# Optimization experiments

Hardware: AMD Instinct MI355X
Metric: run time of the kernel (lower is better)

## Reference

```python
import jax, jax.numpy as jnp
import numpy as np

FM = 80            # feature_maps
N_ROUNDS = 32
NORM_EPS = 1e-3
LOSS_EPS = 1e-8


def _relu6(x):
    return jnp.clip(x, 0.0, 6.0)


def _norm(x):
    # tf.nn.moments over axis 0 + batch_normalization (no scale/offset)
    mean = jnp.mean(x, axis=0, keepdims=True)
    var = jnp.var(x, axis=0, keepdims=True)
    return (x - mean) * jax.lax.rsqrt(var + NORM_EPS)


def setup_inputs() -> dict:
    key = jax.random.key(0)
    n_vars, n_clauses, n_graphs, lits_per_clause = 100000, 420000, 100, 3
    n_cells = n_clauses * lits_per_clause
    ks = jax.random.split(key, 24)

    lit_var = jax.random.randint(ks[0], (n_cells,), 0, n_vars, dtype=jnp.int32)
    lit_neg = jax.random.randint(ks[1], (n_cells,), 0, 2, dtype=jnp.int32)
    clause_idx = jnp.repeat(jnp.arange(n_clauses, dtype=jnp.int32), lits_per_clause)
    clause_graph = jnp.repeat(jnp.arange(n_graphs, dtype=jnp.int32), n_clauses // n_graphs)

    def dense(k, fi, fo):
        return jax.random.normal(k, (fi, fo), jnp.float32) / np.sqrt(fi)

    inp = dict(
        lit_var=lit_var, lit_neg=lit_neg, clause_idx=clause_idx, clause_graph=clause_graph,
        n_vars=n_vars, n_clauses=n_clauses, n_graphs=n_graphs,
        L_init_scale=jnp.float32(1.0 / np.sqrt(FM)),
        C_init_scale=jnp.float32(1.0 / np.sqrt(FM)),
        LC_scale=jnp.float32(0.1), CL_scale=jnp.float32(0.1),
        # L_update MLP: in=3*FM (L, CL_msgs, flip(L)) -> hidden 3*FM relu6 -> FM
        Lu_W0=dense(ks[2], 3 * FM, 3 * FM), Lu_b0=jnp.zeros((3 * FM,), jnp.float32),
        Lu_W1=dense(ks[3], 3 * FM, FM),     Lu_b1=jnp.zeros((FM,), jnp.float32),
        # C_update MLP: in=2*FM (C, LC_msgs) -> hidden 2*FM relu6 -> FM
        Cu_W0=dense(ks[4], 2 * FM, 2 * FM), Cu_b0=jnp.zeros((2 * FM,), jnp.float32),
        Cu_W1=dense(ks[5], 2 * FM, FM),     Cu_b1=jnp.zeros((FM,), jnp.float32),
        # V_score MLP: in=2*FM -> 3 hidden relu6 layers of 2*FM -> 1
        Vs_W0=dense(ks[6], 2 * FM, 2 * FM), Vs_b0=jnp.zeros((2 * FM,), jnp.float32),
        Vs_W1=dense(ks[7], 2 * FM, 2 * FM), Vs_b1=jnp.zeros((2 * FM,), jnp.float32),
        Vs_W2=dense(ks[8], 2 * FM, 2 * FM), Vs_b2=jnp.zeros((2 * FM,), jnp.float32),
        Vs_W3=dense(ks[9], 2 * FM, 1),      Vs_b3=jnp.zeros((1,), jnp.float32),
    )
    return inp


def reference(lit_var, lit_neg, clause_idx, clause_graph, n_vars, n_clauses, n_graphs,
              L_init_scale, C_init_scale, LC_scale, CL_scale,
              Lu_W0, Lu_b0, Lu_W1, Lu_b1,
              Cu_W0, Cu_b0, Cu_W1, Cu_b1,
              Vs_W0, Vs_b0, Vs_W1, Vs_b1, Vs_W2, Vs_b2, Vs_W3, Vs_b3):
    n_lits = 2 * n_vars
    lit_row = lit_var + lit_neg * n_vars          # row in L for each cell
    sign = (1 - 2 * lit_neg).astype(jnp.float32)  # +1 positive literal, -1 negated

    def mlp_L(x):
        return _relu6(x @ Lu_W0 + Lu_b0) @ Lu_W1 + Lu_b1

    def mlp_C(x):
        return _relu6(x @ Cu_W0 + Cu_b0) @ Cu_W1 + Cu_b1

    def v_score(x):
        h = _relu6(x @ Vs_W0 + Vs_b0)
        h = _relu6(h @ Vs_W1 + Vs_b1)
        h = _relu6(h @ Vs_W2 + Vs_b2)
        return h @ Vs_W3 + Vs_b3

    def flip(L):
        return jnp.concatenate([L[n_vars:], L[:n_vars]], axis=0)

    def per_round_loss(logits):
        # softplus_mixed_loss over ragged clauses of signed literals
        lit_vals = logits[lit_var, 0] * sign                         # [n_cells]
        clause_sum = jax.ops.segment_sum(jax.nn.softplus(lit_vals), clause_idx,
                                         num_segments=n_clauses)     # [n_clauses]
        vc = jnp.exp(-clause_sum)
        per_clause = vc * (-jnp.log(1.0 - vc + LOSS_EPS))
        per_graph = jax.ops.segment_sum(per_clause, clause_graph, num_segments=n_graphs)
        return jnp.sum(jnp.sqrt(per_graph + 1e-6))

    L0 = jnp.ones((n_lits, FM), jnp.float32) * L_init_scale
    C0 = jnp.ones((n_clauses, FM), jnp.float32) * C_init_scale

    def round_fn(carry, _):
        L, C, loss = carry
        # CL^T @ L  (sparse gather + segment-sum over clause cells)
        LC_msgs = jax.ops.segment_sum(L[lit_row], clause_idx, num_segments=n_clauses) * LC_scale
        C = _norm(mlp_C(jnp.concatenate([C, LC_msgs], axis=-1)))
        # adj @ C  (scatter-add clause features back to literal rows)
        CL_msgs = jax.ops.segment_sum(C[clause_idx], lit_row, num_segments=n_lits) * CL_scale
        L = _norm(mlp_L(jnp.concatenate([L, CL_msgs, flip(L)], axis=-1)))
        V = jnp.concatenate([L[:n_vars], L[n_vars:]], axis=1)        # [n_vars, 2*FM]
        logits = v_score(V)
        loss = loss + per_round_loss(logits)
        return (L, C, loss), None

    (L, C, loss), _ = jax.lax.scan(round_fn, (L0, C0, jnp.float32(0.0)), None, length=N_ROUNDS)
    # final-round logits (recomputed from the final L state, identical math)
    logits = v_score(jnp.concatenate([L[:n_vars], L[n_vars:]], axis=1))
    return logits, loss / N_ROUNDS
```

## Files before the change

### kernel.cpp

```cpp
#include <hip/hip_runtime.h>
#include <hip/hip_fp8.h>
#include <math.h>


#define NROUNDS 32
#define NORM_EPS 1e-3f
#define LOSS_EPS 1e-8f

static constexpr int NV_CONST = 100000;
static constexpr int NG_CONST = 100;

typedef __attribute__((ext_vector_type(8))) short short8;
typedef __attribute__((ext_vector_type(8))) unsigned char uchar8;
typedef __attribute__((ext_vector_type(16))) unsigned char uchar16;
typedef __attribute__((ext_vector_type(4))) float f32x4;

__device__ __forceinline__ short f2bf(float f) {
    union { float f; unsigned u; } x; x.f = f;
    unsigned r = x.u + 0x7fffu + ((x.u >> 16) & 1u);
    return (short)(r >> 16);
}
__device__ __forceinline__ float bf2f(short s) {
    union { unsigned u; float f; } x; x.u = ((unsigned)(unsigned short)s) << 16;
    return x.f;
}
__device__ __forceinline__ unsigned char f2q8(float f) {
    f = fminf(fmaxf(f, -448.f), 448.f);
    __hip_fp8_e4m3 t(f);
    return t.__x;
}
__device__ __forceinline__ float q82f(unsigned char b) {
    __hip_fp8_e4m3 t; t.__x = b;
    return (float)t;
}


__global__ void k_zero_i(int* __restrict__ p, int n) {
    int i = blockIdx.x * 256 + threadIdx.x;
    if (i < n) p[i] = 0;
}
__global__ void k_fill_b(short* __restrict__ p, int n, const float* __restrict__ vp) {
    int i = blockIdx.x * 256 + threadIdx.x;
    if (i < n) p[i] = f2bf(*vp);
}
__global__ void k_fill_q8(unsigned char* __restrict__ p, int n, const float* __restrict__ vp) {
    int i = blockIdx.x * 256 + threadIdx.x;
    if (i < n) p[i] = f2q8(*vp);
}
__global__ void k_copy_int(int* __restrict__ dst, const int* __restrict__ src, int n) {
    int i = blockIdx.x * 256 + threadIdx.x;
    if (i < n) dst[i] = src[i];
}
__global__ void k_init_slabs(float* __restrict__ slabC, float* __restrict__ slabL,
                             float* __restrict__ loss_a, float nclf, float nlf) {
    int i = blockIdx.x * 256 + threadIdx.x;
    if (i < 33 * 160) {
        slabC[i] = (i >= 80 && i < 160) ? nclf * (1.f - NORM_EPS) : 0.f;
        slabL[i] = (i >= 80 && i < 160) ? nlf * (1.f - NORM_EPS) : 0.f;
    }
    if (i == 0) loss_a[0] = 0.f;
}

__global__ void k_litrow(const int* __restrict__ lit_var, const int* __restrict__ lit_neg,
                         int* __restrict__ litrow, int* __restrict__ lofs4,
                         int* __restrict__ cellpk,
                         int* __restrict__ counts, int ncell, int nv) {
    int i = blockIdx.x * 256 + threadIdx.x;
    if (i < ncell) {
        int vv = lit_var[i], ng = lit_neg[i];
        int r = vv + ng * nv;
        litrow[i] = r;
        int cl = i / 3, t = i - cl * 3;
        lofs4[cl * 4 + t] = r * 8;
        cellpk[i] = vv | (ng << 31);
        atomicAdd(&counts[r], 1);
    }
}

__launch_bounds__(1024)
__global__ void k_scan4(const int* __restrict__ counts, int* __restrict__ row_ptr,
                        int n, int total) {
    __shared__ int sd[1024];
    __shared__ int carry;
    int tid = threadIdx.x;
    if (tid == 0) carry = 0;
    __syncthreads();
    for (int base = 0; base < n; base += 4096) {
        int i0 = base + tid * 4;
        int a0 = (i0 + 0 < n) ? counts[i0 + 0] : 0;
        int a1 = (i0 + 1 < n) ? counts[i0 + 1] : 0;
        int a2 = (i0 + 2 < n) ? counts[i0 + 2] : 0;
        int a3 = (i0 + 3 < n) ? counts[i0 + 3] : 0;
        int s = a0 + a1 + a2 + a3;
        sd[tid] = s;
        __syncthreads();
        for (int off = 1; off < 1024; off <<= 1) {
            int t = (tid >= off) ? sd[tid - off] : 0;
            __syncthreads();
            sd[tid] += t;
            __syncthreads();
        }
        int excl = carry + sd[tid] - s;
        if (i0 + 0 < n) row_ptr[i0 + 0] = excl;
        if (i0 + 1 < n) row_ptr[i0 + 1] = excl + a0;
        if (i0 + 2 < n) row_ptr[i0 + 2] = excl + a0 + a1;
        if (i0 + 3 < n) row_ptr[i0 + 3] = excl + a0 + a1 + a2;
        __syncthreads();
        if (tid == 0) carry += sd[1023];
        __syncthreads();
    }
    if (tid == 0) row_ptr[n] = total;
}

__global__ void k_fill_csr(const int* __restrict__ litrow, const int* __restrict__ clause_idx,
                           int* __restrict__ cursor, int* __restrict__ cl_of, int ncell) {
    int i = blockIdx.x * 256 + threadIdx.x;
    if (i < ncell) {
        int r = litrow[i];
        int pos = atomicAdd(&cursor[r], 1);
        cl_of[pos] = clause_idx[i];
    }
}

__global__ void k_pack_w(const float* __restrict__ W, short* __restrict__ Wp,
                         int K, int N, int KB, int NB) {
    int t = blockIdx.x * 256 + threadIdx.x;
    int tot = NB * KB * 64;
    if (t >= tot) return;
    int lane = t & 63;
    int kb = (t >> 6) % KB;
    int nb = t / (64 * KB);
    int quad = lane >> 4, l15 = lane & 15;
    int n = nb * 16 + l15;
#pragma unroll
    for (int j = 0; j < 8; ++j) {
        int k = kb * 32 + quad * 8 + j;
        float f = (k < K && n < N) ? W[(size_t)k * N + n] : 0.f;
        Wp[(size_t)t * 8 + j] = f2bf(f);
    }
}


template <int KB, int NB>
__device__ __forceinline__ void mfma_layer(const short* lds, int SK,
                                           const short8* __restrict__ Wp,
                                           f32x4* acc, int lane, int arow) {
    const int quad8 = (lane >> 4) * 8;
    short8 a[KB];
#pragma unroll
    for (int kb = 0; kb < KB; ++kb)
        a[kb] = *(const short8*)(lds + arow * SK + kb * 32 + quad8);
#pragma unroll
    for (int kb = 0; kb < KB; ++kb)
#pragma unroll
        for (int nb = 0; nb < NB; ++nb)
            acc[nb] = __builtin_amdgcn_mfma_f32_16x16x32_bf16(
                a[kb], Wp[(nb * KB + kb) * 64 + lane], acc[nb], 0, 0, 0);
}

template <int NB>
__device__ __forceinline__ void write_hidden(short* ldsH, int SKH, const f32x4* acc,
                                             const float* __restrict__ bias,
                                             int l15, int quad, int wr0) {
#pragma unroll
    for (int nb = 0; nb < NB; ++nb) {
        int c = nb * 16 + l15;
        float bv = bias[c];
#pragma unroll
        for (int reg = 0; reg < 4; ++reg) {
            int row = wr0 + quad * 4 + reg;
            float v = acc[nb][reg] + bv;
            v = fminf(fmaxf(v, 0.f), 6.f);
            ldsH[row * SKH + c] = f2bf(v);
        }
    }
}

__device__ __forceinline__ void load_stats(const float* __restrict__ slab, float Minv,
                                           float* sS, int tid) {
    if (tid < 80) {
        float m = slab[tid] * Minv;
        float v = slab[80 + tid] * Minv - m * m;
        sS[tid] = m;
        sS[80 + tid] = rsqrtf(v + NORM_EPS);
    }
}

__launch_bounds__(256, 2)
__global__ void k_c_update(short* __restrict__ Cb, unsigned char* __restrict__ Cb8,
                           const unsigned char* __restrict__ Lb8,
                           const int4* __restrict__ lofs4, const float* __restrict__ scp,
                           const short8* __restrict__ W0p, const float* __restrict__ b0,
                           const short8* __restrict__ W1p, const float* __restrict__ b1,
                           const float* __restrict__ prevSlab, float* __restrict__ nextSlab,
                           float Minv, int ncl) {
    constexpr int SK = 168;
    __shared__ short lds[64 * SK];
    __shared__ float sred[160], sC[160];
    const int lane = threadIdx.x, wy = threadIdx.y, tid = wy * 64 + lane;
    const int r0 = blockIdx.x * 64;
    const int rows = (ncl - r0 < 64) ? (ncl - r0) : 64;

    if (tid < 160) sred[tid] = 0.f;
    load_stats(prevSlab, Minv, sC, tid);
    __syncthreads();

    const float s = *scp;
    const short8* Cbv = (const short8*)Cb;
    const uchar16* Lq = (const uchar16*)Lb8;

#pragma unroll
    for (int u = 0; u < 3; ++u) {
        int it = tid + u * 256;
        int itc = (it < 640) ? it : 639;
        int lr = itc / 10, c = itc - lr * 10;
        int cl = r0 + ((lr < rows) ? lr : rows - 1);
        short8 v = __builtin_nontemporal_load(&Cbv[(size_t)cl * 10 + c]);
        int col = c * 8;
        short8 o;
#pragma unroll
        for (int j = 0; j < 8; ++j)
            o[j] = f2bf((bf2f(v[j]) - sC[col + j]) * sC[80 + col + j]);
        if (it < 640)
            *(short8*)(lds + lr * SK + col) = o;
    }
#pragma unroll
    for (int u = 0; u < 2; ++u) {
        int it = tid + u * 256;
        int itc = (it < 320) ? it : 319;
        int lr = itc / 5, cc = itc - lr * 5;
        int cl = r0 + ((lr < rows) ? lr : rows - 1);
        int4 o4 = lofs4[cl];
        uchar16 va = Lq[(size_t)o4.x + cc];
        uchar16 vb = Lq[(size_t)o4.y + cc];
        uchar16 vc = Lq[(size_t)o4.z + cc];
        short8 o0, o1;
#pragma unroll
        for (int j = 0; j < 8; ++j) {
            o0[j] = f2bf((q82f(va[j]) + q82f(vb[j]) + q82f(vc[j])) * s);
            o1[j] = f2bf((q82f(va[8 + j]) + q82f(vb[8 + j]) + q82f(vc[8 + j])) * s);
        }
        if (it < 320) {
            *(short8*)(lds + lr * SK + 80 + cc * 16) = o0;
            *(short8*)(lds + lr * SK + 80 + cc * 16 + 8) = o1;
        }
    }
    __syncthreads();

    const int quad = lane >> 4, l15 = lane & 15, wr0 = wy * 16, arow = wr0 + l15;

    f32x4 acc[10];
#pragma unroll
    for (int nb = 0; nb < 10; ++nb) { f32x4 z = {0.f, 0.f, 0.f, 0.f}; acc[nb] = z; }
    mfma_layer<5, 10>(lds, SK, W0p, acc, lane, arow);
    write_hidden<10>(lds, SK, acc, b0, l15, quad, wr0);

    f32x4 acc2[5];
#pragma unroll
    for (int nb = 0; nb < 5; ++nb) { f32x4 z = {0.f, 0.f, 0.f, 0.f}; acc2[nb] = z; }
    mfma_layer<5, 5>(lds, SK, W1p, acc2, lane, arow);

#pragma unroll
    for (int nb = 0; nb < 5; ++nb) {
        int cc = nb * 16 + l15;
        float bv = b1[cc];
        float s1 = 0.f, s2 = 0.f;
#pragma unroll
        for (int reg = 0; reg < 4; ++reg) {
            int lr = wr0 + quad * 4 + reg;
            if (lr < rows) {
                float v = acc2[nb][reg] + bv;
                __builtin_nontemporal_store(f2bf(v), &Cb[(size_t)(r0 + lr) * 80 + cc]);
                Cb8[(size_t)(r0 + lr) * 128 + cc] = f2q8(v);
                s1 += v; s2 += v * v;
            }
        }
        s1 += __shfl_xor(s1, 16); s1 += __shfl_xor(s1, 32);
        s2 += __shfl_xor(s2, 16); s2 += __shfl_xor(s2, 32);
        if (quad == 0) { atomicAdd(&sred[cc], s1); atomicAdd(&sred[80 + cc], s2); }
    }
    __syncthreads();
    if (tid < 160) atomicAdd(&nextSlab[tid], sred[tid]);
}

__launch_bounds__(256)
__global__ void k_cl_gather(const unsigned char* __restrict__ Cb8,
                            const int* __restrict__ row_ptr,
                            const int* __restrict__ cl_of, const float* __restrict__ scp,
                            const float* __restrict__ slab, float Minv,
                            short* __restrict__ CLb, int nl) {
    __shared__ float sC[160];
    load_stats(slab, Minv, sC, threadIdx.x);
    __syncthreads();
    int idx = blockIdx.x * 256 + threadIdx.x;
    if (idx >= nl * 5) return;
    int r = idx / 5, c16 = idx - r * 5;
    int p0 = row_ptr[r], p1 = row_ptr[r + 1];
    float a[16];
#pragma unroll
    for (int j = 0; j < 16; ++j) a[j] = 0.f;
    const uchar16* Cq = (const uchar16*)Cb8;
    int p = p0;
    for (; p + 4 <= p1; p += 4) {
        int i0 = cl_of[p], i1 = cl_of[p + 1], i2 = cl_of[p + 2], i3 = cl_of[p + 3];
        uchar16 v0 = Cq[(size_t)i0 * 8 + c16];
        uchar16 v1 = Cq[(size_t)i1 * 8 + c16];
        uchar16 v2 = Cq[(size_t)i2 * 8 + c16];
        uchar16 v3 = Cq[(size_t)i3 * 8 + c16];
#pragma unroll
        for (int j = 0; j < 16; ++j)
            a[j] += (q82f(v0[j]) + q82f(v1[j])) + (q82f(v2[j]) + q82f(v3[j]));
    }
    for (; p < p1; ++p) {
        uchar16 v = Cq[(size_t)cl_of[p] * 8 + c16];
#pragma unroll
        for (int j = 0; j < 16; ++j) a[j] += q82f(v[j]);
    }
    float n = (float)(p1 - p0), s = *scp;
    int col = c16 * 16;
    short8 o0, o1;
#pragma unroll
    for (int j = 0; j < 8; ++j) {
        o0[j] = f2bf((a[j] - n * sC[col + j]) * sC[80 + col + j] * s);
        o1[j] = f2bf((a[8 + j] - n * sC[col + 8 + j]) * sC[80 + col + 8 + j] * s);
    }
    ((short8*)CLb)[(size_t)r * 10 + c16 * 2] = o0;
    ((short8*)CLb)[(size_t)r * 10 + c16 * 2 + 1] = o1;
}

__launch_bounds__(256, 2)
__global__ void k_l_update(short* __restrict__ Lraw, const short* __restrict__ CLb,
                           const short8* __restrict__ W0p, const float* __restrict__ b0,
                           const short8* __restrict__ W1p, const float* __restrict__ b1,
                           const float* __restrict__ prevSlab, float* __restrict__ nextSlab,
                           float Minv, int nv) {
    constexpr int SK = 264;
    __shared__ short lds[64 * SK];
    __shared__ float sred[160], sL[160];
    const int lane = threadIdx.x, wy = threadIdx.y, tid = wy * 64 + lane;
    const int vb = blockIdx.x * 32;

    if (tid < 160) sred[tid] = 0.f;
    load_stats(prevSlab, Minv, sL, tid);
    __syncthreads();

    const short8* Lr8  = (const short8*)Lraw;
    const short8* CLb8 = (const short8*)CLb;
    short8 vals[8];
#pragma unroll
    for (int u = 0; u < 8; ++u) {
        int it = tid + u * 256;
        int lr = it >> 5, c = it & 31;
        int own = (lr < 32) ? vb + lr : vb + nv + (lr - 32);
        int opp = (lr < 32) ? vb + nv + lr : vb + (lr - 32);
        if (c < 10) {
            vals[u] = Lr8[(size_t)own * 10 + c];
        } else if (c < 20) {
            vals[u] = CLb8[(size_t)own * 10 + (c - 10)];
        } else if (c < 30) {
            vals[u] = Lr8[(size_t)opp * 10 + (c - 20)];
        } else {
            short8 z = {0, 0, 0, 0, 0, 0, 0, 0};
            vals[u] = z;
        }
    }
#pragma unroll
    for (int u = 0; u < 8; ++u) {
        int it = tid + u * 256;
        int lr = it >> 5, c = it & 31;
        short8 w = vals[u];
        if (c < 10 || (c >= 20 && c < 30)) {
            int base = (c < 10) ? c * 8 : (c - 20) * 8;
#pragma unroll
            for (int j = 0; j < 8; ++j)
                w[j] = f2bf((bf2f(w[j]) - sL[base + j]) * sL[80 + base + j]);
        }
        int o = (c < 10) ? c * 8 : (c < 20) ? 80 + (c - 10) * 8
              : (c < 30) ? 160 + (c - 20) * 8 : 240 + (c - 30) * 8;
        *(short8*)(lds + lr * SK + o) = w;
    }
    __syncthreads();

    const int quad = lane >> 4, l15 = lane & 15, wr0 = wy * 16, arow = wr0 + l15;

    f32x4 acc[15];
#pragma unroll
    for (int nb = 0; nb < 15; ++nb) { f32x4 z = {0.f, 0.f, 0.f, 0.f}; acc[nb] = z; }
    mfma_layer<8, 15>(lds, SK, W0p, acc, lane, arow);
    write_hidden<15>(lds, SK, acc, b0, l15, quad, wr0);
    {
        int row = wr0 + (lane >> 2);
        int c = 240 + (lane & 3) * 4;
        short4 z; z.x = 0; z.y = 0; z.z = 0; z.w = 0;
        *(short4*)(lds + row * SK + c) = z;
    }

    f32x4 acc2[5];
#pragma unroll
    for (int nb = 0; nb < 5; ++nb) { f32x4 z = {0.f, 0.f, 0.f, 0.f}; acc2[nb] = z; }
    mfma_layer<8, 5>(lds, SK, W1p, acc2, lane, arow);

#pragma unroll
    for (int nb = 0; nb < 5; ++nb) {
        int cc = nb * 16 + l15;
        float bv = b1[cc];
        float s1 = 0.f, s2 = 0.f;
#pragma unroll
        for (int reg = 0; reg < 4; ++reg) {
            int lr = wr0 + quad * 4 + reg;
            int rabs = (lr < 32) ? vb + lr : vb + nv + (lr - 32);
            float v = acc2[nb][reg] + bv;
            Lraw[(size_t)rabs * 80 + cc] = f2bf(v);
            s1 += v; s2 += v * v;
        }
        s1 += __shfl_xor(s1, 16); s1 += __shfl_xor(s1, 32);
        s2 += __shfl_xor(s2, 16); s2 += __shfl_xor(s2, 32);
        if (quad == 0) { atomicAdd(&sred[cc], s1); atomicAdd(&sred[80 + cc], s2); }
    }
    __syncthreads();
    if (tid < 160) atomicAdd(&nextSlab[tid], sred[tid]);
}

__launch_bounds__(256, 2)
__global__ void k_v_head(const short* __restrict__ Lraw, const float* __restrict__ slab,
                         float Minv,
                         const short8* __restrict__ W0p, const float* __restrict__ b0,
                         const short8* __restrict__ W1p, const float* __restrict__ b1,
                         const short8* __restrict__ W2p, const float* __restrict__ b2,
                         const float* __restrict__ W3, const float* __restrict__ b3,
                         float* __restrict__ logits,
                         unsigned char* __restrict__ Lb8, int nv) {
    constexpr int SK = 168;
    __shared__ short lds[64 * SK];
    __shared__ float sW3[160], sL[160];
    const int lane = threadIdx.x, wy = threadIdx.y, tid = wy * 64 + lane;
    const int v0 = blockIdx.x * 64;
    const int cnt = (nv - v0 < 64) ? (nv - v0) : 64;

    if (tid < 160) sW3[tid] = W3[tid];
    load_stats(slab, Minv, sL, tid);
    __syncthreads();

    const short8* Lraw8 = (const short8*)Lraw;
    short8 vals[5];
#pragma unroll
    for (int u = 0; u < 5; ++u) {
        int it = tid + u * 256;
        int lr = it / 20, c = it - lr * 20;
        int v = v0 + ((lr < cnt) ? lr : cnt - 1);
        int row = (c < 10) ? v : v + nv;
        int cc = (c < 10) ? c : c - 10;
        vals[u] = Lraw8[(size_t)row * 10 + cc];
    }
#pragma unroll
    for (int u = 0; u < 5; ++u) {
        int it = tid + u * 256;
        int lr = it / 20, c = it - lr * 20;
        int v = v0 + ((lr < cnt) ? lr : cnt - 1);
        int cc = (c < 10) ? c : c - 10;
        int col = cc * 8;
        short8 o;
        uchar8 q;
#pragma unroll
        for (int j = 0; j < 8; ++j) {
            float f = (bf2f(vals[u][j]) - sL[col + j]) * sL[80 + col + j];
            o[j] = f2bf(f);
            q[j] = f2q8(f);
        }
        *(short8*)(lds + lr * SK + c * 8) = o;
        if (lr < cnt) {
            int lit = (c < 10) ? v : (v + nv);
            *(uchar8*)(Lb8 + (size_t)lit * 128 + cc * 8) = q;
        }
    }
    __syncthreads();

    const int quad = lane >> 4, l15 = lane & 15, wr0 = wy * 16, arow = wr0 + l15;

    f32x4 acc[10];
#pragma unroll
    for (int nb = 0; nb < 10; ++nb) { f32x4 z = {0.f, 0.f, 0.f, 0.f}; acc[nb] = z; }
    mfma_layer<5, 10>(lds, SK, W0p, acc, lane, arow);
    write_hidden<10>(lds, SK, acc, b0, l15, quad, wr0);

#pragma unroll
    for (int nb = 0; nb < 10; ++nb) { f32x4 z = {0.f, 0.f, 0.f, 0.f}; acc[nb] = z; }
    mfma_layer<5, 10>(lds, SK, W1p, acc, lane, arow);
    write_hidden<10>(lds, SK, acc, b1, l15, quad, wr0);

#pragma unroll
    for (int nb = 0; nb < 10; ++nb) { f32x4 z = {0.f, 0.f, 0.f, 0.f}; acc[nb] = z; }
    mfma_layer<5, 10>(lds, SK, W2p, acc, lane, arow);
    write_hidden<10>(lds, SK, acc, b2, l15, quad, wr0);
    __syncthreads();

    int lrow = tid >> 2, t4 = tid & 3;
    float v = 0.f;
    for (int c = t4; c < 160; c += 4) v += bf2f(lds[lrow * SK + c]) * sW3[c];
    v += __shfl_down(v, 2, 4);
    v += __shfl_down(v, 1, 4);
    if (t4 == 0 && lrow < cnt) logits[v0 + lrow] = v + b3[0];
}

__device__ __forceinline__ float softplusf(float x) {
    return fmaxf(x, 0.f) + log1pf(expf(-fabsf(x)));
}

__global__ void k_loss(const float* __restrict__ logits, const int* __restrict__ cellpk,
                       float* __restrict__ loss_acc, int cpg) {
    const int g = blockIdx.x;
    const int tid = threadIdx.x;
    float part = 0.f;
    int cend = (g + 1) * cpg;
    for (int c = g * cpg + tid; c < cend; c += 256) {
        float cs = 0.f;
#pragma unroll
        for (int t = 0; t < 3; ++t) {
            int cp = cellpk[c * 3 + t];
            float sign = (cp < 0) ? -1.f : 1.f;
            cs += softplusf(logits[cp & 0x7fffffff] * sign);
        }
        float vc = expf(-cs);
        part += vc * (-log1pf(LOSS_EPS - vc));
    }
    __shared__ float red[256];
    red[tid] = part;
    __syncthreads();
    for (int s = 128; s > 0; s >>= 1) {
        if (tid < s) red[tid] += red[tid + s];
        __syncthreads();
    }
    if (tid == 0) atomicAdd(loss_acc, sqrtf(red[0] + 1e-6f));
}

__global__ void k_output(float* __restrict__ dout, const float* __restrict__ logits,
                         const float* __restrict__ loss_acc, int nv) {
    int i = blockIdx.x * 256 + threadIdx.x;
    if (i < nv) dout[i] = logits[i];
    else if (i == nv) dout[i] = loss_acc[0] * (1.f / (float)NROUNDS);
}


extern "C" void kernel_launch(void* const* d_in, const int* in_sizes, int n_in,
                              void* d_out, int out_size, void* d_ws, size_t ws_size,
                              hipStream_t stream) {
    const int* lit_var    = (const int*)d_in[0];
    const int* lit_neg    = (const int*)d_in[1];
    const int* clause_idx = (const int*)d_in[2];
    const float* Lscale = (const float*)d_in[7];
    const float* Cscale = (const float*)d_in[8];
    const float* LCs    = (const float*)d_in[9];
    const float* CLs    = (const float*)d_in[10];
    const float* LuW0 = (const float*)d_in[11]; const float* Lub0 = (const float*)d_in[12];
    const float* LuW1 = (const float*)d_in[13]; const float* Lub1 = (const float*)d_in[14];
    const float* CuW0 = (const float*)d_in[15]; const float* Cub0 = (const float*)d_in[16];
    const float* CuW1 = (const float*)d_in[17]; const float* Cub1 = (const float*)d_in[18];
    const float* VsW0 = (const float*)d_in[19]; const float* Vsb0 = (const float*)d_in[20];
    const float* VsW1 = (const float*)d_in[21]; const float* Vsb1 = (const float*)d_in[22];
    const float* VsW2 = (const float*)d_in[23]; const float* Vsb2 = (const float*)d_in[24];
    const float* VsW3 = (const float*)d_in[25]; const float* Vsb3 = (const float*)d_in[26];

    const int ncell = in_sizes[0];
    const int ncl   = in_sizes[3];
    const int nv    = NV_CONST;
    const int nl    = 2 * nv;
    const int ng    = NG_CONST;

    size_t off = 0;
    auto A = [&](size_t bytes) -> void* {
        void* q = (char*)d_ws + off;
        off = (off + bytes + 255) & ~(size_t)255;
        return q;
    };
    short* Cb    = (short*)A((size_t)ncl * 80 * 2);
    short* Lraw  = (short*)A((size_t)nl * 80 * 2);
    short* CLb   = (short*)A((size_t)nl * 80 * 2);
    unsigned char* Lb8 = (unsigned char*)A((size_t)nl * 128);
    unsigned char* Cb8 = (unsigned char*)A((size_t)ncl * 128);
    float* logits = (float*)A((size_t)nv * 4);
    float* slabC  = (float*)A(33 * 160 * 4);
    float* slabL  = (float*)A(33 * 160 * 4);
    float* loss_a = (float*)A(256);
    int* litrow  = (int*)A((size_t)ncell * 4);
    int* lofs4   = (int*)A((size_t)ncl * 16);
    int* cellpk  = (int*)A((size_t)ncell * 4);
    int* row_ptr = (int*)A((size_t)(nl + 1) * 4);
    int* tmp     = (int*)A((size_t)nl * 4);
    int* cl_of   = (int*)A((size_t)ncell * 4);
    short* CuW0p = (short*)A((size_t)10 * 5 * 64 * 16);
    short* CuW1p = (short*)A((size_t)5  * 5 * 64 * 16);
    short* LuW0p = (short*)A((size_t)15 * 8 * 64 * 16);
    short* LuW1p = (short*)A((size_t)5  * 8 * 64 * 16);
    short* VsW0p = (short*)A((size_t)10 * 5 * 64 * 16);
    short* VsW1p = (short*)A((size_t)10 * 5 * 64 * 16);
    short* VsW2p = (short*)A((size_t)10 * 5 * 64 * 16);

    const dim3 B64x4(64, 4, 1);

    k_zero_i<<<(nl + 255) / 256, 256, 0, stream>>>(tmp, nl);
    k_init_slabs<<<(33 * 160 + 255) / 256, 256, 0, stream>>>(slabC, slabL, loss_a,
                                                             (float)ncl, (float)nl);
    k_litrow<<<(ncell + 255) / 256, 256, 0, stream>>>(lit_var, lit_neg, litrow, lofs4,
                                                      cellpk, tmp, ncell, nv);
    k_scan4<<<1, 1024, 0, stream>>>(tmp, row_ptr, nl, ncell);
    k_copy_int<<<(nl + 255) / 256, 256, 0, stream>>>(tmp, row_ptr, nl);
    k_fill_csr<<<(ncell + 255) / 256, 256, 0, stream>>>(litrow, clause_idx, tmp, cl_of, ncell);
    k_fill_b<<<(ncl * 80 + 255) / 256, 256, 0, stream>>>(Cb, ncl * 80, Cscale);
    k_fill_b<<<(nl * 80 + 255) / 256, 256, 0, stream>>>(Lraw, nl * 80, Lscale);
    k_fill_q8<<<(nl * 128 + 255) / 256, 256, 0, stream>>>(Lb8, nl * 128, Lscale);
    k_fill_q8<<<(ncl * 128 + 255) / 256, 256, 0, stream>>>(Cb8, ncl * 128, Cscale);
    k_pack_w<<<(10 * 5 * 64 + 255) / 256, 256, 0, stream>>>(CuW0, CuW0p, 160, 160, 5, 10);
    k_pack_w<<<(5  * 5 * 64 + 255) / 256, 256, 0, stream>>>(CuW1, CuW1p, 160, 80, 5, 5);
    k_pack_w<<<(15 * 8 * 64 + 255) / 256, 256, 0, stream>>>(LuW0, LuW0p, 240, 240, 8, 15);
    k_pack_w<<<(5  * 8 * 64 + 255) / 256, 256, 0, stream>>>(LuW1, LuW1p, 240, 80, 8, 5);
    k_pack_w<<<(10 * 5 * 64 + 255) / 256, 256, 0, stream>>>(VsW0, VsW0p, 160, 160, 5, 10);
    k_pack_w<<<(10 * 5 * 64 + 255) / 256, 256, 0, stream>>>(VsW1, VsW1p, 160, 160, 5, 10);
    k_pack_w<<<(10 * 5 * 64 + 255) / 256, 256, 0, stream>>>(VsW2, VsW2p, 160, 160, 5, 10);

    const int cblk  = (ncl + 63) / 64;
    const int lblk  = nv / 32;
    const int vblk  = (nv + 63) / 64;
    const int clblk = (nl * 5 + 255) / 256;
    const float MinvC = 1.f / (float)ncl;
    const float MinvL = 1.f / (float)nl;

    for (int r = 0; r < NROUNDS; ++r) {
        float* sCr  = slabC + (size_t)r * 160;
        float* sCr1 = slabC + (size_t)(r + 1) * 160;
        float* sLr  = slabL + (size_t)r * 160;
        float* sLr1 = slabL + (size_t)(r + 1) * 160;
        k_c_update<<<cblk, B64x4, 0, stream>>>(
            Cb, Cb8, Lb8, (const int4*)lofs4, LCs, (const short8*)CuW0p, Cub0,
            (const short8*)CuW1p, Cub1, sCr, sCr1, MinvC, ncl);
        k_cl_gather<<<clblk, 256, 0, stream>>>(Cb8, row_ptr, cl_of, CLs, sCr1, MinvC, CLb, nl);
        k_l_update<<<lblk, B64x4, 0, stream>>>(
            Lraw, CLb, (const short8*)LuW0p, Lub0, (const short8*)LuW1p, Lub1,
            sLr, sLr1, MinvL, nv);
        k_v_head<<<vblk, B64x4, 0, stream>>>(
            Lraw, sLr1, MinvL, (const short8*)VsW0p, Vsb0, (const short8*)VsW1p, Vsb1,
            (const short8*)VsW2p, Vsb2, VsW3, Vsb3, logits, Lb8, nv);
        k_loss<<<ng, 256, 0, stream>>>(logits, cellpk, loss_a, ncl / ng);
    }

    k_output<<<(nv + 1 + 255) / 256, 256, 0, stream>>>((float*)d_out, logits, loss_a, nv);
}
```

Measured before the change: 15.54 ms.

## Reorder clauses by first literal and swizzle blocks across XCDs

```diff
diff --git a/kernel.cpp b/kernel.cpp
--- a/kernel.cpp
+++ b/kernel.cpp
@@ -34,6 +34,12 @@
     return (float)t;
 }
 
+__device__ __forceinline__ int xcd_swz(int b, int nb) {
+    int q = nb >> 3, r = nb & 7;
+    int xcd = b & 7, idx = b >> 3;
+    return (xcd < r ? xcd * (q + 1) : r * (q + 1) + (xcd - r) * q) + idx;
+}
+
 
 __global__ void k_zero_i(int* __restrict__ p, int n) {
     int i = blockIdx.x * 256 + threadIdx.x;
@@ -62,18 +68,17 @@
 }
 
 __global__ void k_litrow(const int* __restrict__ lit_var, const int* __restrict__ lit_neg,
-                         int* __restrict__ litrow, int* __restrict__ lofs4,
-                         int* __restrict__ cellpk,
-                         int* __restrict__ counts, int ncell, int nv) {
+                         int* __restrict__ litrow, int* __restrict__ cellpk,
+                         int* __restrict__ counts, int* __restrict__ fhist,
+                         int ncell, int nv) {
     int i = blockIdx.x * 256 + threadIdx.x;
     if (i < ncell) {
         int vv = lit_var[i], ng = lit_neg[i];
         int r = vv + ng * nv;
         litrow[i] = r;
-        int cl = i / 3, t = i - cl * 3;
-        lofs4[cl * 4 + t] = r * 8;
         cellpk[i] = vv | (ng << 31);
         atomicAdd(&counts[r], 1);
+        if (i % 3 == 0) atomicAdd(&fhist[r], 1);
     }
 }
 
@@ -112,13 +117,27 @@
     if (tid == 0) row_ptr[n] = total;
 }
 
+__global__ void k_place(const int* __restrict__ litrow, int* __restrict__ fcur,
+                        int* __restrict__ newpos, int* __restrict__ lofs4, int ncl) {
+    int c = blockIdx.x * 256 + threadIdx.x;
+    if (c < ncl) {
+        int k = litrow[3 * c];
+        int np = atomicAdd(&fcur[k], 1);
+        newpos[c] = np;
+        lofs4[np * 4 + 0] = litrow[3 * c + 0] * 8;
+        lofs4[np * 4 + 1] = litrow[3 * c + 1] * 8;
+        lofs4[np * 4 + 2] = litrow[3 * c + 2] * 8;
+    }
+}
+
 __global__ void k_fill_csr(const int* __restrict__ litrow, const int* __restrict__ clause_idx,
+                           const int* __restrict__ newpos,
                            int* __restrict__ cursor, int* __restrict__ cl_of, int ncell) {
     int i = blockIdx.x * 256 + threadIdx.x;
     if (i < ncell) {
         int r = litrow[i];
         int pos = atomicAdd(&cursor[r], 1);
-        cl_of[pos] = clause_idx[i];
+        cl_of[pos] = newpos[clause_idx[i]];
     }
 }
 
@@ -198,7 +217,7 @@
     __shared__ short lds[64 * SK];
     __shared__ float sred[160], sC[160];
     const int lane = threadIdx.x, wy = threadIdx.y, tid = wy * 64 + lane;
-    const int r0 = blockIdx.x * 64;
+    const int r0 = xcd_swz(blockIdx.x, gridDim.x) * 64;
     const int rows = (ncl - r0 < 64) ? (ncl - r0) : 64;
 
     if (tid < 160) sred[tid] = 0.f;
@@ -292,7 +311,7 @@
     __shared__ float sC[160];
     load_stats(slab, Minv, sC, threadIdx.x);
     __syncthreads();
-    int idx = blockIdx.x * 256 + threadIdx.x;
+    int idx = xcd_swz(blockIdx.x, gridDim.x) * 256 + threadIdx.x;
     if (idx >= nl * 5) return;
     int r = idx / 5, c16 = idx - r * 5;
     int p0 = row_ptr[r], p1 = row_ptr[r + 1];
@@ -587,6 +606,9 @@
     int* row_ptr = (int*)A((size_t)(nl + 1) * 4);
     int* tmp     = (int*)A((size_t)nl * 4);
     int* cl_of   = (int*)A((size_t)ncell * 4);
+    int* fhist   = (int*)A((size_t)nl * 4);
+    int* fbase   = (int*)A((size_t)(nl + 1) * 4);
+    int* newpos  = (int*)A((size_t)ncl * 4);
     short* CuW0p = (short*)A((size_t)10 * 5 * 64 * 16);
     short* CuW1p = (short*)A((size_t)5  * 5 * 64 * 16);
     short* LuW0p = (short*)A((size_t)15 * 8 * 64 * 16);
@@ -598,13 +620,18 @@
     const dim3 B64x4(64, 4, 1);
 
     k_zero_i<<<(nl + 255) / 256, 256, 0, stream>>>(tmp, nl);
+    k_zero_i<<<(nl + 255) / 256, 256, 0, stream>>>(fhist, nl);
     k_init_slabs<<<(33 * 160 + 255) / 256, 256, 0, stream>>>(slabC, slabL, loss_a,
                                                              (float)ncl, (float)nl);
-    k_litrow<<<(ncell + 255) / 256, 256, 0, stream>>>(lit_var, lit_neg, litrow, lofs4,
-                                                      cellpk, tmp, ncell, nv);
+    k_litrow<<<(ncell + 255) / 256, 256, 0, stream>>>(lit_var, lit_neg, litrow, cellpk,
+                                                      tmp, fhist, ncell, nv);
     k_scan4<<<1, 1024, 0, stream>>>(tmp, row_ptr, nl, ncell);
+    k_scan4<<<1, 1024, 0, stream>>>(fhist, fbase, nl, ncl);
     k_copy_int<<<(nl + 255) / 256, 256, 0, stream>>>(tmp, row_ptr, nl);
-    k_fill_csr<<<(ncell + 255) / 256, 256, 0, stream>>>(litrow, clause_idx, tmp, cl_of, ncell);
+    k_copy_int<<<(nl + 255) / 256, 256, 0, stream>>>(fhist, fbase, nl);
+    k_place<<<(ncl + 255) / 256, 256, 0, stream>>>(litrow, fhist, newpos, lofs4, ncl);
+    k_fill_csr<<<(ncell + 255) / 256, 256, 0, stream>>>(litrow, clause_idx, newpos,
+                                                        tmp, cl_of, ncell);
     k_fill_b<<<(ncl * 80 + 255) / 256, 256, 0, stream>>>(Cb, ncl * 80, Cscale);
     k_fill_b<<<(nl * 80 + 255) / 256, 256, 0, stream>>>(Lraw, nl * 80, Lscale);
     k_fill_q8<<<(nl * 128 + 255) / 256, 256, 0, stream>>>(Lb8, nl * 128, Lscale);
```

After: 15.79 ms. Within noise of the previous version (+1.6%).
